# Kernel tuning notes

Measured on AMD Instinct MI355X. Metric: run time of the kernel, lower is better.

The kernel has to match this reference:

```python
import jax, jax.numpy as jnp
import numpy as np

B, LQ, LD, H, DIM, PF = 16, 64, 2048, 1024, 128, 4
MAXK = LD // PF + 1  # static upper bound on num clusters (valid_len <= LD)


def setup_inputs() -> dict:
    key = jax.random.key(0)
    k1, k2, k3, k4 = jax.random.split(key, 4)
    return {
        "q_hidden": jax.random.normal(k1, (B, LQ, H), jnp.float32),
        "d_hidden": jax.random.normal(k2, (B, LD, H), jnp.float32),
        "W": jax.random.normal(k3, (H, DIM), jnp.float32) * (1.0 / np.sqrt(H)),  # xavier-ish
        "b": jnp.zeros((DIM,), jnp.float32),
        "q_mask": jnp.ones((B, LQ), jnp.int32),
        "d_mask": jnp.ones((B, LD), jnp.int32),
        "labels": jax.random.randint(k4, (B, LD), 0, MAXK, dtype=jnp.int32),
        "pooling_factor": PF,
    }


def _encode(hidden, W, b, mask):
    # proj -> L2 normalize -> zero out padded tokens
    r = hidden @ W + b
    r = r / jnp.clip(jnp.linalg.norm(r, axis=-1, keepdims=True), 1e-12)
    return r * mask[..., None].astype(r.dtype)


def _pool(d_repr, d_mask, labels, pf):
    # segment-mean per batch sample, cluster labels supplied externally
    Bn, L, D = d_repr.shape
    max_k = L // pf + 1  # static
    valid = jnp.clip(d_mask.sum(-1), 2, None)          # [B]
    k = valid // pf + 1                                 # per-sample num clusters
    lab = jnp.where(d_mask > 0, labels % k[:, None], max_k)  # invalid tokens -> dummy seg
    seg = lambda vals, idx: jax.ops.segment_sum(vals, idx, num_segments=max_k + 1)
    sums = jax.vmap(seg)(d_repr, lab)[:, :max_k]                          # [B,K,D]
    counts = jax.vmap(seg)(jnp.where(d_mask > 0, 1.0, 0.0), lab)[:, :max_k]
    means = sums / jnp.clip(counts, 1.0)[..., None]
    means = means / jnp.clip(jnp.linalg.norm(means, axis=-1, keepdims=True), 1e-12)
    pad_mask = jnp.arange(max_k)[None, :] < k[:, None]                    # [B,K]
    return means * pad_mask[..., None], pad_mask


def reference(q_hidden, d_hidden, W, b, q_mask, d_mask, labels, pooling_factor):
    q = _encode(q_hidden, W, b, q_mask)            # [B,LQ,DIM]
    d = _encode(d_hidden, W, b, d_mask)            # [B,LD,DIM]
    d_pool, pmask = _pool(d, d_mask, labels, pooling_factor)  # [B,K,DIM]
    sim = jnp.einsum('bqd,bkd->bqk', q, d_pool)
    sim = jnp.where(pmask[:, None, :], sim, -1e4)
    score = (sim.max(-1) * q_mask.astype(sim.dtype)).sum(-1)  # maxsum per pair
    return score
```

## Files before the change

### kernel.cpp

```cpp
#include <hip/hip_runtime.h>
#include <hip/hip_bf16.h>

#define BB    16
#define LQ    64
#define LD    2048
#define HH    1024
#define DIM   128
#define MAXK  513
#define SCH   9
#define DGRID 1024
#define QGRID 32

typedef __attribute__((ext_vector_type(8))) short short8;
typedef __attribute__((ext_vector_type(4))) float f32x4;

__device__ __forceinline__ float b2f(ushort u) {
    union { float f; unsigned int u32; } c; c.u32 = ((unsigned int)u) << 16; return c.f;
}
__device__ __forceinline__ ushort f2b_rn(float f) {
    unsigned int x = __float_as_uint(f);
    return (ushort)((x + 0x7fffu + ((x >> 16) & 1u)) >> 16);
}

__device__ __forceinline__ void gld16(void* lds, const void* g) {
    __builtin_amdgcn_global_load_lds(
        (const __attribute__((address_space(1))) unsigned int*)g,
        (__attribute__((address_space(3))) unsigned int*)lds,
        16, 0, 0);
}

__global__ __launch_bounds__(256) void prep_kb_kernel(
    const float* __restrict__ W,
    const int*   __restrict__ d_mask,
    const int*   __restrict__ pf,
    ushort*      __restrict__ Wt,
    int*         __restrict__ kvals,
    float*       __restrict__ sums)
{
    int bid = blockIdx.x, t = threadIdx.x;
    if (bid < 16) {
        __shared__ ushort tile[128][72];
        const int h0 = bid * 64;
        #pragma unroll
        for (int i = 0; i < 32; ++i) {
            int flat = i * 256 + t;
            int r = flat >> 7, c = flat & 127;
            tile[c][r] = f2b_rn(W[(long)(h0 + r) * DIM + c]);
        }
        __syncthreads();
        #pragma unroll
        for (int i = 0; i < 4; ++i) {
            int flat = i * 256 + t;
            int n = flat >> 3, u = flat & 7;
            uint4 v = *(const uint4*)&tile[n][u * 8];
            *(uint4*)&Wt[(long)n * HH + h0 + u * 8] = v;
        }
    } else if (bid < 32) {
        __shared__ int red[4];
        int b = bid - 16;
        int lane = t & 63, wave = t >> 6;
        int s = 0;
        for (int i = t; i < LD; i += 256) s += (d_mask[b * LD + i] > 0) ? 1 : 0;
        #pragma unroll
        for (int m = 1; m < 64; m <<= 1) s += __shfl_xor(s, m);
        if (lane == 0) red[wave] = s;
        __syncthreads();
        if (t == 0) {
            int v = red[0] + red[1] + red[2] + red[3];
            if (v < 2) v = 2;
            int pfv = pf[0];
            if (pfv < 1 || pfv > LD) pfv = 4;
            kvals[b] = v / pfv + 1;
        }
    } else {
        const int total4 = (BB * MAXK * DIM) / 4;
        float4* s4 = (float4*)sums;
        const float4 z = make_float4(0.f, 0.f, 0.f, 0.f);
        for (int i = (bid - 32) * 256 + t; i < total4; i += 256 * 256)
            s4[i] = z;
    }
}

__global__ __launch_bounds__(256, 3) void encode_kernel(
    const float*  __restrict__ Xd,
    const float*  __restrict__ Xq,
    const ushort* __restrict__ Wt,
    const float*  __restrict__ bias,
    const int*    __restrict__ mask_d,
    const int*    __restrict__ mask_q,
    const int*    __restrict__ labels,
    const int*    __restrict__ kvals,
    float*        __restrict__ sums,
    float*        __restrict__ q_repr)
{
    __shared__ __align__(16) uint4 buf[4][768];
    __shared__ float ssh[32][2];

    const int bid = blockIdx.x;
    const bool isq = bid >= DGRID;
    const float* X = isq ? Xq : Xd;
    const long row0 = isq ? (long)(bid - DGRID) * 32 : (long)bid * 32;

    const int t = threadIdx.x;
    const int w = t >> 6, lane = t & 63;
    const int m16 = lane & 15, quad = lane >> 4;
    const int rh = w & 1, ch = w >> 1;

    const float*  gA  = X + (row0 + w * 8 + (lane >> 3)) * HH
                          + (((lane & 7) ^ ((lane >> 3) & 7)) * 4);
    const ushort* gB0 = Wt + (long)(w * 32 + (lane >> 2)) * HH
                           + (((lane & 3) ^ ((lane >> 4) & 3)) * 8);
    const ushort* gB1 = gB0 + 16 * HH;

    f32x4 acc[4];
    #pragma unroll
    for (int j = 0; j < 4; ++j) acc[j] = (f32x4){0.f, 0.f, 0.f, 0.f};

    #pragma unroll
    for (int p = 0; p < 3; ++p) {
        const int ko = p * 32;
        gld16(&buf[p][w * 64], gA + ko);
        gld16(&buf[p][256 + w * 128], gB0 + ko);
        gld16(&buf[p][256 + w * 128 + 64], gB1 + ko);
    }

    const int sw = m16 & 7;
    const int bsw = m16 >> 2;
    const int au = (rh * 16 + m16) * 8;

    auto compute = [&](int cur) {
        float4 va0 = *(const float4*)&buf[cur][au + ((2 * quad) ^ sw)];
        float4 va1 = *(const float4*)&buf[cur][au + ((2 * quad + 1) ^ sw)];
        float av[8];
        *(float4*)(av) = va0; *(float4*)(av + 4) = va1;
        short8 ah, al;
        #pragma unroll
        for (int j = 0; j < 8; ++j) {
            unsigned int ux = __float_as_uint(av[j]);
            ah[j] = (short)(ux >> 16);
            float hif = __uint_as_float(ux & 0xffff0000u);
            al[j] = (short)(__float_as_uint(av[j] - hif) >> 16);
        }
        #pragma unroll
        for (int cti = 0; cti < 4; ++cti) {
            const int ct = ch * 4 + cti;
            short8 bf = *(const short8*)&buf[cur][256 + (ct * 16 + m16) * 4 + (quad ^ bsw)];
            acc[cti] = __builtin_amdgcn_mfma_f32_16x16x32_bf16(ah, bf, acc[cti], 0, 0, 0);
            acc[cti] = __builtin_amdgcn_mfma_f32_16x16x32_bf16(al, bf, acc[cti], 0, 0, 0);
        }
    };

    for (int c = 0; c < 29; ++c) {
        asm volatile("s_waitcnt vmcnt(6)" ::: "memory");
        __builtin_amdgcn_s_barrier();
        __builtin_amdgcn_sched_barrier(0);
        const int nxt = (c + 3) & 3;
        const int ko = (c + 3) * 32;
        gld16(&buf[nxt][w * 64], gA + ko);
        gld16(&buf[nxt][256 + w * 128], gB0 + ko);
        gld16(&buf[nxt][256 + w * 128 + 64], gB1 + ko);
        compute(c & 3);
    }
    asm volatile("s_waitcnt vmcnt(6)" ::: "memory");
    __builtin_amdgcn_s_barrier();
    __builtin_amdgcn_sched_barrier(0);
    compute(1);
    asm volatile("s_waitcnt vmcnt(3)" ::: "memory");
    __builtin_amdgcn_s_barrier();
    __builtin_amdgcn_sched_barrier(0);
    compute(2);
    asm volatile("s_waitcnt vmcnt(0)" ::: "memory");
    __builtin_amdgcn_s_barrier();
    __builtin_amdgcn_sched_barrier(0);
    compute(3);

    float bia[4];
    #pragma unroll
    for (int cti = 0; cti < 4; ++cti) bia[cti] = bias[(ch * 4 + cti) * 16 + m16];

    float vv[4][4];
    float ssp[4] = {0.f, 0.f, 0.f, 0.f};
    #pragma unroll
    for (int cti = 0; cti < 4; ++cti)
        #pragma unroll
        for (int r = 0; r < 4; ++r) {
            vv[cti][r] = acc[cti][r] + bia[cti];
            ssp[r] += vv[cti][r] * vv[cti][r];
        }
    #pragma unroll
    for (int r = 0; r < 4; ++r) {
        ssp[r] += __shfl_xor(ssp[r], 1);
        ssp[r] += __shfl_xor(ssp[r], 2);
        ssp[r] += __shfl_xor(ssp[r], 4);
        ssp[r] += __shfl_xor(ssp[r], 8);
    }
    if (m16 == 0) {
        #pragma unroll
        for (int r = 0; r < 4; ++r) ssh[rh * 16 + quad * 4 + r][ch] = ssp[r];
    }
    __syncthreads();

    #pragma unroll
    for (int r = 0; r < 4; ++r) {
        int rowl = rh * 16 + quad * 4 + r;
        long rowg = row0 + rowl;
        float ss = ssh[rowl][0] + ssh[rowl][1];
        float scale = 1.0f / fmaxf(sqrtf(ss), 1e-12f);
        if (isq) {
            scale *= (float)mask_q[rowg];
            #pragma unroll
            for (int cti = 0; cti < 4; ++cti)
                q_repr[rowg * DIM + (ch * 4 + cti) * 16 + m16] = vv[cti][r] * scale;
        } else if (mask_d[rowg] > 0) {
            int b = (int)(rowg >> 11);
            int seg = labels[rowg] % kvals[b];
            float* sp = sums + ((long)b * MAXK + seg) * DIM + m16;
            #pragma unroll
            for (int cti = 0; cti < 4; ++cti)
                atomicAdd(sp + (ch * 4 + cti) * 16, vv[cti][r] * scale);
        }
    }
}

__global__ __launch_bounds__(256) void simmax_kernel(
    const float* __restrict__ q_repr,
    const float* __restrict__ sums,
    const int*   __restrict__ kvals,
    float*       __restrict__ pmax)
{
    __shared__ __align__(16) ushort Qh[64 * 136];
    __shared__ __align__(16) ushort Ql[64 * 136];
    __shared__ __align__(16) ushort Ch[64 * 136];
    __shared__ float cn[64];

    int b = blockIdx.x / SCH, chunk = blockIdx.x % SCH;
    int t = threadIdx.x, w = t >> 6, lane = t & 63;
    int m16 = lane & 15, quad = lane >> 4;

    #pragma unroll
    for (int i = 0; i < 8; ++i) {
        int flat = i * 256 + t;
        int row = flat >> 5, c4 = flat & 31;
        float4 v = *(const float4*)(q_repr + ((long)b * LQ + row) * DIM + c4 * 4);
        float x[4]; *(float4*)x = v;
        ushort4 h, l;
        ushort* hp = (ushort*)&h; ushort* lp = (ushort*)&l;
        #pragma unroll
        for (int j = 0; j < 4; ++j) {
            unsigned int ux = __float_as_uint(x[j]);
            hp[j] = (ushort)(ux >> 16);
            lp[j] = f2b_rn(x[j] - __uint_as_float(ux & 0xffff0000u));
        }
        *(ushort4*)&Qh[row * 136 + c4 * 4] = h;
        *(ushort4*)&Ql[row * 136 + c4 * 4] = l;
    }
    #pragma unroll
    for (int i = 0; i < 8; ++i) {
        int flat = i * 256 + t;
        int row = flat >> 5, c4 = flat & 31;
        int kk = chunk * 64 + row;
        float4 v = (kk < MAXK)
            ? *(const float4*)(sums + ((long)b * MAXK + kk) * DIM + c4 * 4)
            : make_float4(0.f, 0.f, 0.f, 0.f);
        ushort4 h; ushort* hp = (ushort*)&h;
        hp[0] = f2b_rn(v.x); hp[1] = f2b_rn(v.y);
        hp[2] = f2b_rn(v.z); hp[3] = f2b_rn(v.w);
        *(ushort4*)&Ch[row * 136 + c4 * 4] = h;
    }
    __syncthreads();

    {
        int c = w * 16 + m16;
        float ssv = 0.f;
        #pragma unroll
        for (int j = 0; j < 16; ++j) {
            unsigned int u = *(const unsigned int*)&Ch[c * 136 + quad * 32 + j * 2];
            float x0 = b2f((ushort)u), x1 = b2f((ushort)(u >> 16));
            ssv += x0 * x0 + x1 * x1;
        }
        ssv += __shfl_xor(ssv, 16);
        ssv += __shfl_xor(ssv, 32);
        if (quad == 0) cn[c] = (ssv > 1e-24f) ? rsqrtf(ssv) : 0.f;
    }
    __syncthreads();

    f32x4 acc[4];
    #pragma unroll
    for (int j = 0; j < 4; ++j) acc[j] = (f32x4){0.f, 0.f, 0.f, 0.f};

    #pragma unroll
    for (int kc = 0; kc < 4; ++kc) {
        short8 qh = *(const short8*)&Qh[(w * 16 + m16) * 136 + kc * 32 + quad * 8];
        short8 ql = *(const short8*)&Ql[(w * 16 + m16) * 136 + kc * 32 + quad * 8];
        #pragma unroll
        for (int ct = 0; ct < 4; ++ct) {
            short8 cf = *(const short8*)&Ch[(ct * 16 + m16) * 136 + kc * 32 + quad * 8];
            acc[ct] = __builtin_amdgcn_mfma_f32_16x16x32_bf16(qh, cf, acc[ct], 0, 0, 0);
            acc[ct] = __builtin_amdgcn_mfma_f32_16x16x32_bf16(ql, cf, acc[ct], 0, 0, 0);
        }
    }

    int kb = kvals[b];
    #pragma unroll
    for (int r = 0; r < 4; ++r) {
        float mx = -1e4f;
        #pragma unroll
        for (int ct = 0; ct < 4; ++ct) {
            int cl = chunk * 64 + ct * 16 + m16;
            float sim = acc[ct][r] * cn[ct * 16 + m16];
            mx = fmaxf(mx, (cl < kb) ? sim : -1e4f);
        }
        mx = fmaxf(mx, __shfl_xor(mx, 1));
        mx = fmaxf(mx, __shfl_xor(mx, 2));
        mx = fmaxf(mx, __shfl_xor(mx, 4));
        mx = fmaxf(mx, __shfl_xor(mx, 8));
        if (m16 == 0)
            pmax[((long)b * SCH + chunk) * 64 + w * 16 + quad * 4 + r] = mx;
    }
}

__global__ __launch_bounds__(64) void final_kernel(
    const float* __restrict__ pmax,
    const int*   __restrict__ q_mask,
    float*       __restrict__ out)
{
    int b = blockIdx.x, r = threadIdx.x;
    float m = -3e38f;
    #pragma unroll
    for (int c = 0; c < SCH; ++c)
        m = fmaxf(m, pmax[((long)b * SCH + c) * 64 + r]);
    m *= (float)q_mask[b * LQ + r];
    #pragma unroll
    for (int sh = 1; sh < 64; sh <<= 1) m += __shfl_xor(m, sh);
    if (r == 0) out[b] = m;
}

extern "C" void kernel_launch(void* const* d_in, const int* in_sizes, int n_in,
                              void* d_out, int out_size, void* d_ws, size_t ws_size,
                              hipStream_t stream) {
    const float* q_hidden = (const float*)d_in[0];
    const float* d_hidden = (const float*)d_in[1];
    const float* W        = (const float*)d_in[2];
    const float* bias     = (const float*)d_in[3];
    const int*   q_mask   = (const int*)d_in[4];
    const int*   d_mask   = (const int*)d_in[5];
    const int*   labels   = (const int*)d_in[6];
    const int*   pf       = (const int*)d_in[7];

    float* ws     = (float*)d_ws;
    float* q_repr = ws;
    float* sums   = q_repr + (long)BB * LQ * DIM;
    float* pmaxb  = sums + (long)BB * MAXK * DIM;
    int*   kvals  = (int*)(pmaxb + BB * SCH * 64);
    ushort* Wt    = (ushort*)(kvals + 16);

    prep_kb_kernel<<<288, 256, 0, stream>>>(W, d_mask, pf, Wt, kvals, sums);
    encode_kernel<<<DGRID + QGRID, 256, 0, stream>>>(d_hidden, q_hidden, Wt, bias,
                                                     d_mask, q_mask, labels, kvals,
                                                     sums, q_repr);
    simmax_kernel<<<BB * SCH, 256, 0, stream>>>(q_repr, sums, kvals, pmaxb);
    final_kernel<<<BB, 64, 0, stream>>>(pmaxb, q_mask, (float*)d_out);
}
```

Baseline: 265.9 us.

## Enlarge encode tile to 64 rows with 512 threads and 3-stage buffering

The encode GEMM now runs 512-thread blocks, each covering 64 rows instead of 32, which halves the grid. With more rows per block, each loaded W tile is reused across twice as many rows. The cp.async-style LDS pipeline drops from 4 buffers with 3 tiles in flight to 3 buffers with 2 in flight, and the main loop is unrolled in steps of three. The shallower prefetch depth and the larger block may reduce latency hiding and occupancy. The epilogue, not fully shown, must handle 64 rows and 8 waves correctly.

```diff
diff --git a/kernel.cpp b/kernel.cpp
--- a/kernel.cpp
+++ b/kernel.cpp
@@ -8,8 +8,8 @@
 #define DIM   128
 #define MAXK  513
 #define SCH   9
-#define DGRID 1024
-#define QGRID 32
+#define DGRID 512
+#define QGRID 16
 
 typedef __attribute__((ext_vector_type(8))) short short8;
 typedef __attribute__((ext_vector_type(4))) float f32x4;
@@ -81,7 +81,7 @@
     }
 }
 
-__global__ __launch_bounds__(256, 3) void encode_kernel(
+__global__ __launch_bounds__(512, 6) void encode_kernel(
     const float*  __restrict__ Xd,
     const float*  __restrict__ Xq,
     const ushort* __restrict__ Wt,
@@ -93,44 +93,43 @@
     float*        __restrict__ sums,
     float*        __restrict__ q_repr)
 {
-    __shared__ __align__(16) uint4 buf[4][768];
-    __shared__ float ssh[32][2];
+    __shared__ __align__(16) uint4 buf[3][1024];
+    __shared__ float ssh[64][2];
 
     const int bid = blockIdx.x;
     const bool isq = bid >= DGRID;
     const float* X = isq ? Xq : Xd;
-    const long row0 = isq ? (long)(bid - DGRID) * 32 : (long)bid * 32;
+    const long row0 = isq ? (long)(bid - DGRID) * 64 : (long)bid * 64;
 
     const int t = threadIdx.x;
     const int w = t >> 6, lane = t & 63;
     const int m16 = lane & 15, quad = lane >> 4;
-    const int rh = w & 1, ch = w >> 1;
-
-    const float*  gA  = X + (row0 + w * 8 + (lane >> 3)) * HH
-                          + (((lane & 7) ^ ((lane >> 3) & 7)) * 4);
-    const ushort* gB0 = Wt + (long)(w * 32 + (lane >> 2)) * HH
-                           + (((lane & 3) ^ ((lane >> 4) & 3)) * 8);
-    const ushort* gB1 = gB0 + 16 * HH;
+    const int rh = w & 3, ch = w >> 2;
+
+    const float*  gA = X + (row0 + w * 8 + (lane >> 3)) * HH
+                         + (((lane & 7) ^ ((lane >> 3) & 7)) * 4);
+    const ushort* gB = Wt + (long)(w * 16 + (lane >> 2)) * HH
+                          + (((lane & 3) ^ ((lane >> 4) & 3)) * 8);
+
+    const int wA = w * 64;
+    const int wB = 512 + w * 64;
 
     f32x4 acc[4];
     #pragma unroll
     for (int j = 0; j < 4; ++j) acc[j] = (f32x4){0.f, 0.f, 0.f, 0.f};
 
-    #pragma unroll
-    for (int p = 0; p < 3; ++p) {
-        const int ko = p * 32;
-        gld16(&buf[p][w * 64], gA + ko);
-        gld16(&buf[p][256 + w * 128], gB0 + ko);
-        gld16(&buf[p][256 + w * 128 + 64], gB1 + ko);
-    }
+    gld16(&buf[0][wA], gA);
+    gld16(&buf[0][wB], gB);
+    gld16(&buf[1][wA], gA + 32);
+    gld16(&buf[1][wB], gB + 32);
 
     const int sw = m16 & 7;
     const int bsw = m16 >> 2;
     const int au = (rh * 16 + m16) * 8;
 
-    auto compute = [&](int cur) {
-        float4 va0 = *(const float4*)&buf[cur][au + ((2 * quad) ^ sw)];
-        float4 va1 = *(const float4*)&buf[cur][au + ((2 * quad + 1) ^ sw)];
+    auto compute = [&](const uint4* bb) {
+        float4 va0 = *(const float4*)&bb[au + ((2 * quad) ^ sw)];
+        float4 va1 = *(const float4*)&bb[au + ((2 * quad + 1) ^ sw)];
         float av[8];
         *(float4*)(av) = va0; *(float4*)(av + 4) = va1;
         short8 ah, al;
@@ -144,35 +143,34 @@
         #pragma unroll
         for (int cti = 0; cti < 4; ++cti) {
             const int ct = ch * 4 + cti;
-            short8 bf = *(const short8*)&buf[cur][256 + (ct * 16 + m16) * 4 + (quad ^ bsw)];
+            short8 bf = *(const short8*)&bb[512 + (ct * 16 + m16) * 4 + (quad ^ bsw)];
             acc[cti] = __builtin_amdgcn_mfma_f32_16x16x32_bf16(ah, bf, acc[cti], 0, 0, 0);
             acc[cti] = __builtin_amdgcn_mfma_f32_16x16x32_bf16(al, bf, acc[cti], 0, 0, 0);
         }
     };
 
-    for (int c = 0; c < 29; ++c) {
-        asm volatile("s_waitcnt vmcnt(6)" ::: "memory");
-        __builtin_amdgcn_s_barrier();
-        __builtin_amdgcn_sched_barrier(0);
-        const int nxt = (c + 3) & 3;
-        const int ko = (c + 3) * 32;
-        gld16(&buf[nxt][w * 64], gA + ko);
-        gld16(&buf[nxt][256 + w * 128], gB0 + ko);
-        gld16(&buf[nxt][256 + w * 128 + 64], gB1 + ko);
-        compute(c & 3);
-    }
-    asm volatile("s_waitcnt vmcnt(6)" ::: "memory");
+    #define STEP(C, CUR, NXT)                                              \
+        asm volatile("s_waitcnt vmcnt(2)" ::: "memory");                   \
+        __builtin_amdgcn_s_barrier();                                      \
+        __builtin_amdgcn_sched_barrier(0);                                 \
+        gld16(&buf[NXT][wA], gA + ((C) + 2) * 32);                         \
+        gld16(&buf[NXT][wB], gB + ((C) + 2) * 32);                         \
+        compute(&buf[CUR][0]);
+
+    for (int c = 0; c < 30; c += 3) {
+        STEP(c + 0, 0, 2)
+        STEP(c + 1, 1, 0)
+        STEP(c + 2, 2, 1)
+    }
+    #undef STEP
+    asm volatile("s_waitcnt vmcnt(2)" ::: "memory");
     __builtin_amdgcn_s_barrier();
     __builtin_amdgcn_sched_barrier(0);
-    compute(1);
-    asm volatile("s_waitcnt vmcnt(3)" ::: "memory");
-    __builtin_amdgcn_s_barrier();
-    __builtin_amdgcn_sched_barrier(0);
-    compute(2);
+    compute(&buf[0][0]);
     asm volatile("s_waitcnt vmcnt(0)" ::: "memory");
     __builtin_amdgcn_s_barrier();
     __builtin_amdgcn_sched_barrier(0);
-    compute(3);
+    compute(&buf[1][0]);
 
     float bia[4];
     #pragma unroll
@@ -355,7 +353,7 @@
     ushort* Wt    = (ushort*)(kvals + 16);
 
     prep_kb_kernel<<<288, 256, 0, stream>>>(W, d_mask, pf, Wt, kvals, sums);
-    encode_kernel<<<DGRID + QGRID, 256, 0, stream>>>(d_hidden, q_hidden, Wt, bias,
+    encode_kernel<<<DGRID + QGRID, 512, 0, stream>>>(d_hidden, q_hidden, Wt, bias,
                                                      d_mask, q_mask, labels, kvals,
                                                      sums, q_repr);
     simmax_kernel<<<BB * SCH, 256, 0, stream>>>(q_repr, sums, kvals, pmaxb);
```

Result: faster. 254.9 us (-4.1%).
